# Optimization experiments

Measured on AMD Instinct MI355X. Metric: run time of the kernel, lower is better.

The kernel has to match this reference:

```python
import jax, jax.numpy as jnp
import numpy as np

PAD = 0
NEG_INF = -1e30

B, P, Q, D = 32, 4096, 64, 128  # batch, passage len, question len, nhid


def setup_inputs() -> dict:
    key = jax.random.key(0)
    k1, k2, k3, k4, k5, k6 = jax.random.split(key, 6)
    return {
        "tensor_H": jax.random.normal(k1, (B, P, D), dtype=jnp.float32),
        "tensor_U": jax.random.normal(k2, (B, Q, D), dtype=jnp.float32),
        "M": jax.random.normal(k3, (B, P, D), dtype=jnp.float32),
        "sentence_word_rep": jax.random.randint(k4, (B, P), 0, 10000, dtype=jnp.int64),
        "W_attn": jax.random.normal(k5, (D, D), dtype=jnp.float32) / np.sqrt(D),
        "W_cls": jax.random.normal(k6, (5 * D, 2), dtype=jnp.float32) / np.sqrt(5 * D),
    }


def reference(tensor_H, tensor_U, M, sentence_word_rep, W_attn, W_cls):
    # Matrix attention (bilinear): S[b,p,q] = h_p^T W u_q  -> (B, P, Q)
    S = jnp.einsum("bpd,de,bqe->bpq", tensor_H, W_attn, tensor_U)
    # context-to-query: softmax over question axis, then bmm with U
    c2q = jnp.einsum("bpq,bqd->bpd", jax.nn.softmax(S, axis=2), tensor_U)
    # query-to-context: softmax over passage axis of row-max, weighted sum of H
    b_attn = jax.nn.softmax(jnp.max(S, axis=2), axis=-1)        # (B, P)
    q2c = jnp.einsum("bp,bpd->bd", b_attn, tensor_H)[:, None, :]  # (B, 1, D) broadcast over P
    # G = [H; c2q; H*c2q; H*q2c] -> (B, P, 4D); G_M = [G; M] -> (B, P, 5D)
    G_M = jnp.concatenate(
        [tensor_H, c2q, tensor_H * c2q, tensor_H * q2c, M], axis=2
    )
    # masked max-pool over passage positions (mask where token == PAD)
    pad_mask = (sentence_word_rep == PAD)[:, :, None]           # (B, P, 1)
    pooled = jnp.max(jnp.where(pad_mask, NEG_INF, G_M), axis=1)  # (B, 5D)
    # final linear classifier (no bias)
    return pooled @ W_cls                                        # (B, 2)
```

## Files before the change

### kernel.cpp

```cpp
#include <hip/hip_runtime.h>

#define B_ 32
#define P_ 4096
#define Q_ 64
#define D_ 128

#define PART_STRIDE 772
#define NCHUNK 32
#define CHUNK_ROWS 128
#define TWS_BYTES (96*16384)

typedef __attribute__((ext_vector_type(8))) short bf16x8;
typedef __attribute__((ext_vector_type(4))) float f32x4;

__device__ __forceinline__ unsigned int asu(float x) { return __float_as_uint(x); }
__device__ __forceinline__ float asf(unsigned int x) { return __uint_as_float(x); }

__global__ __launch_bounds__(256) void k_T(const float* __restrict__ U,
                                           const float* __restrict__ W,
                                           char* __restrict__ Tws) {
  __shared__ float Wl[128*132];
  __shared__ float Ul[8*128];
  const int b = blockIdx.x >> 3, qc = blockIdx.x & 7;
  const int t = threadIdx.x;
#pragma unroll
  for (int k = 0; k < 16; ++k) {
    int i = t*4 + k*1024;
    float4 wv = *(const float4*)(W + i);
    int d = i >> 7, e = i & 127;
    *(float4*)(&Wl[d*132 + e]) = wv;
  }
  {
    int i = t*4;
    int q = i >> 7, e = i & 127;
    *(float4*)(&Ul[q*128 + e]) =
        *(const float4*)(U + ((size_t)(b*Q_ + qc*8 + q))*D_ + e);
  }
  __syncthreads();
  const int d = t & 127, qhalf = t >> 7;
  char* Thi = Tws + b*16384;
  char* Tlo = Tws + 32*16384 + b*16384;
  char* Utl = Tws + 64*16384 + b*16384;
#pragma unroll
  for (int pass = 0; pass < 4; ++pass) {
    const int ql = pass*2 + qhalf;
    const int qg = qc*8 + ql;
    float acc = 0.f;
#pragma unroll
    for (int e = 0; e < 128; e += 4) {
      float4 wv = *(float4*)(&Wl[d*132 + e]);
      float4 uv = *(float4*)(&Ul[ql*128 + e]);
      acc += wv.x*uv.x + wv.y*uv.y + wv.z*uv.z + wv.w*uv.w;
    }
    unsigned int au = asu(acc);
    unsigned short hs = (unsigned short)(au >> 16);
    float lo = acc - asf(au & 0xFFFF0000u);
    unsigned short ls = (unsigned short)(asu(lo) >> 16);
    int ta = (qg*256 + 2*d) ^ ((qg & 7) << 4);
    *(unsigned short*)(Thi + ta) = hs;
    *(unsigned short*)(Tlo + ta) = ls;
    float uval = Ul[ql*128 + d];
    int ua = (d*128 + 2*qg) ^ ((d & 7) << 4);
    *(unsigned short*)(Utl + ua) = (unsigned short)(asu(uval) >> 16);
  }
}

__global__ __launch_bounds__(512, 3) void k_main(
    const float* __restrict__ H, const float* __restrict__ M,
    const int* __restrict__ tok, const char* __restrict__ Tws,
    float* __restrict__ part) {
  __shared__ __align__(16) char Tl[32768];
  __shared__ __align__(16) char Pl[16384];
  __shared__ __align__(16) float mrow[128];
  __shared__ __align__(16) float rzrow[128];
  __shared__ __align__(16) float prow[128];
  __shared__ __align__(16) float bm[128];
  __shared__ int tkl[128];

  const int bid = blockIdx.x;
  const int b = bid >> 5, chunk = bid & 31;
  const int t = threadIdx.x, wv = t >> 6, l = t & 63;
  const int r15 = l & 15, g4 = l >> 4;
  const char* Thi_g = Tws + b*16384;
  const char* Tlo_g = Tws + 32*16384 + b*16384;
  const char* Utl   = Tws + 64*16384 + b*16384;

  const int dA = wv*16 + r15;
  bf16x8 au0 = *(const bf16x8*)(Utl + ((dA*128 + g4*16 +  0) ^ ((dA & 7) << 4)));
  bf16x8 au1 = *(const bf16x8*)(Utl + ((dA*128 + g4*16 + 64) ^ ((dA & 7) << 4)));

  {
    const uint4* sh = (const uint4*)Thi_g;
    const uint4* sl = (const uint4*)Tlo_g;
    uint4* dh = (uint4*)Tl;
    uint4* dl = (uint4*)(Tl + 16384);
    dh[t]       = sh[t];
    dh[t + 512] = sh[t + 512];
    dl[t]       = sl[t];
    dl[t + 512] = sl[t + 512];
  }
  if (t < 128) tkl[t] = tok[b*P_ + chunk*CHUNK_ROWS + t];
  __syncthreads();

  const int rowB = b*P_ + chunk*CHUNK_ROWS;

  {
    const int lrow0 = wv*16;
    const float* Arow = H + (size_t)(rowB + lrow0 + r15)*D_;
    f32x4 fA[4], fB[4];
#pragma unroll
    for (int ks = 0; ks < 4; ++ks) {
      const float* ap = Arow + ks*32 + g4*8;
      fA[ks] = *(const f32x4*)(ap);
      fB[ks] = *(const f32x4*)(ap + 4);
    }
    union { bf16x8 v; unsigned int u[4]; } Ah[4], Al[4];
#pragma unroll
    for (int ks = 0; ks < 4; ++ks) {
      unsigned int a0 = asu(fA[ks][0]), a1 = asu(fA[ks][1]),
                   a2 = asu(fA[ks][2]), a3 = asu(fA[ks][3]);
      unsigned int c0 = asu(fB[ks][0]), c1 = asu(fB[ks][1]),
                   c2 = asu(fB[ks][2]), c3 = asu(fB[ks][3]);
      Ah[ks].u[0] = (a1 & 0xFFFF0000u) | (a0 >> 16);
      Ah[ks].u[1] = (a3 & 0xFFFF0000u) | (a2 >> 16);
      Ah[ks].u[2] = (c1 & 0xFFFF0000u) | (c0 >> 16);
      Ah[ks].u[3] = (c3 & 0xFFFF0000u) | (c2 >> 16);
      float p0 = fA[ks][0] - asf(a0 & 0xFFFF0000u);
      float p1 = fA[ks][1] - asf(a1 & 0xFFFF0000u);
      float p2 = fA[ks][2] - asf(a2 & 0xFFFF0000u);
      float p3 = fA[ks][3] - asf(a3 & 0xFFFF0000u);
      float p4 = fB[ks][0] - asf(c0 & 0xFFFF0000u);
      float p5 = fB[ks][1] - asf(c1 & 0xFFFF0000u);
      float p6 = fB[ks][2] - asf(c2 & 0xFFFF0000u);
      float p7 = fB[ks][3] - asf(c3 & 0xFFFF0000u);
      Al[ks].u[0] = (asu(p1) & 0xFFFF0000u) | (asu(p0) >> 16);
      Al[ks].u[1] = (asu(p3) & 0xFFFF0000u) | (asu(p2) >> 16);
      Al[ks].u[2] = (asu(p5) & 0xFFFF0000u) | (asu(p4) >> 16);
      Al[ks].u[3] = (asu(p7) & 0xFFFF0000u) | (asu(p6) >> 16);
    }
    f32x4 sacc[4];
#pragma unroll
    for (int qt = 0; qt < 4; ++qt) sacc[qt] = (f32x4){0.f, 0.f, 0.f, 0.f};
#pragma unroll
    for (int ks = 0; ks < 4; ++ks) {
#pragma unroll
      for (int qt = 0; qt < 4; ++qt) {
        int q = qt*16 + r15;
        int off = (q*256 + ks*64 + g4*16) ^ ((q & 7) << 4);
        bf16x8 bh = *(const bf16x8*)(Tl + off);
        bf16x8 bl = *(const bf16x8*)(Tl + 16384 + off);
        sacc[qt] = __builtin_amdgcn_mfma_f32_16x16x32_bf16(Al[ks].v, bh, sacc[qt], 0, 0, 0);
        sacc[qt] = __builtin_amdgcn_mfma_f32_16x16x32_bf16(Ah[ks].v, bl, sacc[qt], 0, 0, 0);
        sacc[qt] = __builtin_amdgcn_mfma_f32_16x16x32_bf16(Ah[ks].v, bh, sacc[qt], 0, 0, 0);
      }
    }
    float m[4];
#pragma unroll
    for (int j = 0; j < 4; ++j)
      m[j] = fmaxf(fmaxf(sacc[0][j], sacc[1][j]), fmaxf(sacc[2][j], sacc[3][j]));
#pragma unroll
    for (int off = 1; off <= 8; off <<= 1)
#pragma unroll
      for (int j = 0; j < 4; ++j) m[j] = fmaxf(m[j], __shfl_xor(m[j], off));
    float Zp[4] = {0.f, 0.f, 0.f, 0.f};
#pragma unroll
    for (int qt = 0; qt < 4; ++qt)
#pragma unroll
      for (int j = 0; j < 4; ++j) {
        float e = __expf(sacc[qt][j] - m[j]);
        Zp[j] += e;
        int p = lrow0 + g4*4 + j, q = qt*16 + r15;
        int off = (p*128 + 2*q) ^ ((p & 7) << 4);
        *(unsigned short*)(Pl + off) = (unsigned short)(asu(e) >> 16);
      }
#pragma unroll
    for (int off = 1; off <= 8; off <<= 1)
#pragma unroll
      for (int j = 0; j < 4; ++j) Zp[j] += __shfl_xor(Zp[j], off);
    if (r15 == 0) {
#pragma unroll
      for (int j = 0; j < 4; ++j) {
        mrow[lrow0 + g4*4 + j]  = m[j];
        rzrow[lrow0 + g4*4 + j] = __builtin_amdgcn_rcpf(Zp[j]);
      }
    }
  }
  __syncthreads();

  float m0 = mrow[l], m1 = mrow[l + 64];
  float Lm = fmaxf(m0, m1);
#pragma unroll
  for (int off = 1; off <= 32; off <<= 1) Lm = fmaxf(Lm, __shfl_xor(Lm, off));
  float ssum = __expf(m0 - Lm) + __expf(m1 - Lm);
#pragma unroll
  for (int off = 1; off <= 32; off <<= 1) ssum += __shfl_xor(ssum, off);
  if (t < 128) {
    prow[t] = __expf(mrow[t] - Lm);
    bm[t]   = tkl[t] ? 0.f : -1.0e38f;
  }
  __syncthreads();

  f32x4 v4  = (f32x4){0.f, 0.f, 0.f, 0.f};
  f32x4 xH4 = (f32x4){-3.0e38f, -3.0e38f, -3.0e38f, -3.0e38f};
  f32x4 nH4 = (f32x4){ 3.0e38f,  3.0e38f,  3.0e38f,  3.0e38f};
  f32x4 xC4 = (f32x4){-3.0e38f, -3.0e38f, -3.0e38f, -3.0e38f};
  f32x4 xHC4= (f32x4){-3.0e38f, -3.0e38f, -3.0e38f, -3.0e38f};
  f32x4 xM4 = (f32x4){-3.0e38f, -3.0e38f, -3.0e38f, -3.0e38f};
  const int dbase = wv*16 + g4*4;
#pragma unroll
  for (int rti = 0; rti < 8; ++rti) {
    const int rt = (rti + wv) & 7;
    const int p = rt*16 + r15;
    const int pswz = (p & 7) << 4;
    bf16x8 pb0 = *(bf16x8*)(Pl + ((p*128 + g4*16 +  0) ^ pswz));
    bf16x8 pb1 = *(bf16x8*)(Pl + ((p*128 + g4*16 + 64) ^ pswz));
    f32x4 pv = (f32x4){0.f, 0.f, 0.f, 0.f};
    pv = __builtin_amdgcn_mfma_f32_16x16x32_bf16(au0, pb0, pv, 0, 0, 0);
    pv = __builtin_amdgcn_mfma_f32_16x16x32_bf16(au1, pb1, pv, 0, 0, 0);
    const float prw = prow[p], rz = rzrow[p], bmv = bm[p];
    f32x4 h4 = *(const f32x4*)(H + (size_t)(rowB + p)*D_ + dbase);
    f32x4 m4 = *(const f32x4*)(M + (size_t)(rowB + p)*D_ + dbase);
#pragma unroll
    for (int j = 0; j < 4; ++j) {
      float c = pv[j] * rz;
      v4[j]   += prw*h4[j];
      xH4[j]   = fmaxf(xH4[j],  h4[j] + bmv);
      nH4[j]   = fminf(nH4[j],  h4[j] - bmv);
      xC4[j]   = fmaxf(xC4[j],  c + bmv);
      xHC4[j]  = fmaxf(xHC4[j], h4[j]*c + bmv);
      xM4[j]   = fmaxf(xM4[j],  m4[j] + bmv);
    }
  }
#pragma unroll
  for (int off = 1; off <= 8; off <<= 1) {
#pragma unroll
    for (int j = 0; j < 4; ++j) {
      v4[j]  += __shfl_xor(v4[j], off);
      xH4[j]  = fmaxf(xH4[j],  __shfl_xor(xH4[j],  off));
      nH4[j]  = fminf(nH4[j],  __shfl_xor(nH4[j],  off));
      xC4[j]  = fmaxf(xC4[j],  __shfl_xor(xC4[j],  off));
      xHC4[j] = fmaxf(xHC4[j], __shfl_xor(xHC4[j], off));
      xM4[j]  = fmaxf(xM4[j],  __shfl_xor(xM4[j],  off));
    }
  }
  float* pp = part + (size_t)bid*PART_STRIDE;
  if (t == 0) { pp[0] = Lm; pp[1] = ssum; }
  if (r15 == 0) {
#pragma unroll
    for (int j = 0; j < 4; ++j) {
      pp[2 + dbase + j]   = v4[j];
      pp[130 + dbase + j] = xH4[j];
      pp[258 + dbase + j] = nH4[j];
      pp[386 + dbase + j] = xC4[j];
      pp[514 + dbase + j] = xHC4[j];
      pp[642 + dbase + j] = xM4[j];
    }
  }
}

__global__ __launch_bounds__(128) void k_final(const float* __restrict__ part,
                                               const float* __restrict__ Wc,
                                               float* __restrict__ out) {
  __shared__ float pooled[640];
  __shared__ float r0s[2], r1s[2];
  const int b = blockIdx.x, t = threadIdx.x;
  const float* pb = part + (size_t)b*NCHUNK*PART_STRIDE;
  float L = -3.0e38f;
#pragma unroll
  for (int c = 0; c < NCHUNK; ++c) L = fmaxf(L, pb[c*PART_STRIDE]);
  float S = 0.f, V = 0.f;
  float mh = -3.0e38f, nh = 3.0e38f, mc = -3.0e38f, mhc = -3.0e38f, mm = -3.0e38f;
#pragma unroll
  for (int c = 0; c < NCHUNK; ++c) {
    const float* p = pb + c*PART_STRIDE;
    float e = __expf(p[0] - L);
    S += p[1]*e;
    V += p[2 + t]*e;
    mh  = fmaxf(mh,  p[130 + t]);
    nh  = fminf(nh,  p[258 + t]);
    mc  = fmaxf(mc,  p[386 + t]);
    mhc = fmaxf(mhc, p[514 + t]);
    mm  = fmaxf(mm,  p[642 + t]);
  }
  float q2c = V / S;
  pooled[t]       = mh;
  pooled[128 + t] = mc;
  pooled[256 + t] = mhc;
  pooled[384 + t] = (q2c >= 0.f) ? q2c*mh : q2c*nh;
  pooled[512 + t] = mm;
  __syncthreads();
  float a0 = 0.f, a1 = 0.f;
#pragma unroll
  for (int k = t; k < 640; k += 128) {
    float pv = pooled[k];
    a0 += pv*Wc[k*2 + 0];
    a1 += pv*Wc[k*2 + 1];
  }
#pragma unroll
  for (int off = 32; off; off >>= 1) {
    a0 += __shfl_xor(a0, off);
    a1 += __shfl_xor(a1, off);
  }
  if ((t & 63) == 0) { r0s[t >> 6] = a0; r1s[t >> 6] = a1; }
  __syncthreads();
  if (t == 0) {
    out[b*2 + 0] = r0s[0] + r0s[1];
    out[b*2 + 1] = r1s[0] + r1s[1];
  }
}

extern "C" void kernel_launch(void* const* d_in, const int* in_sizes, int n_in,
                              void* d_out, int out_size, void* d_ws, size_t ws_size,
                              hipStream_t stream) {
  const float* H   = (const float*)d_in[0];
  const float* U   = (const float*)d_in[1];
  const float* M   = (const float*)d_in[2];
  const int*   tok = (const int*)d_in[3];
  const float* Wa  = (const float*)d_in[4];
  const float* Wc  = (const float*)d_in[5];
  float* out = (float*)d_out;
  char* wsc = (char*)d_ws;
  char* Tws = wsc;
  float* part = (float*)(wsc + TWS_BYTES);

  hipLaunchKernelGGL(k_T,     dim3(256),        dim3(256), 0, stream, U, Wa, Tws);
  hipLaunchKernelGGL(k_main,  dim3(B_*NCHUNK),  dim3(512), 0, stream, H, M, tok, Tws, part);
  hipLaunchKernelGGL(k_final, dim3(B_),         dim3(128), 0, stream, part, Wc, out);
}
```

Before: 58.89 us.

## Process two 128-row halves per block to amortize T staging

Doubles the rows handled by each main-kernel block from 128 to 256, so there are half as many blocks. Each block stages the per-batch T matrix into LDS once and runs two interleaved 128-row streams through the MFMA score, softmax and pooling phases. This amortizes the T load and block setup and raises instruction-level parallelism per wave. In exchange it uses more registers and LDS, drops the occupancy hint from 3 to 2 blocks per CU, and launches fewer blocks (512 instead of 1024).

```diff
diff --git a/kernel.cpp b/kernel.cpp
--- a/kernel.cpp
+++ b/kernel.cpp
@@ -6,8 +6,8 @@
 #define D_ 128
 
 #define PART_STRIDE 772
-#define NCHUNK 32
-#define CHUNK_ROWS 128
+#define NCHUNK 16
+#define CHUNK_ROWS 256
 #define TWS_BYTES (96*16384)
 
 typedef __attribute__((ext_vector_type(8))) short bf16x8;
@@ -15,6 +15,30 @@
 
 __device__ __forceinline__ unsigned int asu(float x) { return __float_as_uint(x); }
 __device__ __forceinline__ float asf(unsigned int x) { return __uint_as_float(x); }
+
+__device__ __forceinline__ void repack8(const f32x4 fa, const f32x4 fb,
+                                        bf16x8* hi, bf16x8* lo) {
+  union { bf16x8 v; unsigned int u[4]; } Hh, Ll;
+  unsigned int a0 = asu(fa[0]), a1 = asu(fa[1]), a2 = asu(fa[2]), a3 = asu(fa[3]);
+  unsigned int c0 = asu(fb[0]), c1 = asu(fb[1]), c2 = asu(fb[2]), c3 = asu(fb[3]);
+  Hh.u[0] = (a1 & 0xFFFF0000u) | (a0 >> 16);
+  Hh.u[1] = (a3 & 0xFFFF0000u) | (a2 >> 16);
+  Hh.u[2] = (c1 & 0xFFFF0000u) | (c0 >> 16);
+  Hh.u[3] = (c3 & 0xFFFF0000u) | (c2 >> 16);
+  float p0 = fa[0] - asf(a0 & 0xFFFF0000u);
+  float p1 = fa[1] - asf(a1 & 0xFFFF0000u);
+  float p2 = fa[2] - asf(a2 & 0xFFFF0000u);
+  float p3 = fa[3] - asf(a3 & 0xFFFF0000u);
+  float p4 = fb[0] - asf(c0 & 0xFFFF0000u);
+  float p5 = fb[1] - asf(c1 & 0xFFFF0000u);
+  float p6 = fb[2] - asf(c2 & 0xFFFF0000u);
+  float p7 = fb[3] - asf(c3 & 0xFFFF0000u);
+  Ll.u[0] = (asu(p1) & 0xFFFF0000u) | (asu(p0) >> 16);
+  Ll.u[1] = (asu(p3) & 0xFFFF0000u) | (asu(p2) >> 16);
+  Ll.u[2] = (asu(p5) & 0xFFFF0000u) | (asu(p4) >> 16);
+  Ll.u[3] = (asu(p7) & 0xFFFF0000u) | (asu(p6) >> 16);
+  *hi = Hh.v; *lo = Ll.v;
+}
 
 __global__ __launch_bounds__(256) void k_T(const float* __restrict__ U,
                                            const float* __restrict__ W,
@@ -65,20 +89,21 @@
   }
 }
 
-__global__ __launch_bounds__(512, 3) void k_main(
+__global__ __launch_bounds__(512, 2) void k_main(
     const float* __restrict__ H, const float* __restrict__ M,
     const int* __restrict__ tok, const char* __restrict__ Tws,
     float* __restrict__ part) {
   __shared__ __align__(16) char Tl[32768];
-  __shared__ __align__(16) char Pl[16384];
-  __shared__ __align__(16) float mrow[128];
-  __shared__ __align__(16) float rzrow[128];
-  __shared__ __align__(16) float prow[128];
-  __shared__ __align__(16) float bm[128];
-  __shared__ int tkl[128];
+  __shared__ __align__(16) char PA[16384];
+  __shared__ __align__(16) char PB[16384];
+  __shared__ __align__(16) float mrow[256];
+  __shared__ __align__(16) float rzrow[256];
+  __shared__ __align__(16) float prow[256];
+  __shared__ __align__(16) float bm[256];
+  __shared__ int tkl[256];
 
   const int bid = blockIdx.x;
-  const int b = bid >> 5, chunk = bid & 31;
+  const int b = bid >> 4, chunk = bid & 15;
   const int t = threadIdx.x, wv = t >> 6, l = t & 63;
   const int r15 = l & 15, g4 = l >> 4;
   const char* Thi_g = Tws + b*16384;
@@ -99,48 +124,37 @@
     dl[t]       = sl[t];
     dl[t + 512] = sl[t + 512];
   }
-  if (t < 128) tkl[t] = tok[b*P_ + chunk*CHUNK_ROWS + t];
+  if (t < 256) tkl[t] = tok[b*P_ + chunk*CHUNK_ROWS + t];
   __syncthreads();
 
   const int rowB = b*P_ + chunk*CHUNK_ROWS;
 
   {
     const int lrow0 = wv*16;
-    const float* Arow = H + (size_t)(rowB + lrow0 + r15)*D_;
-    f32x4 fA[4], fB[4];
+    const float* ArowA = H + (size_t)(rowB + lrow0 + r15)*D_;
+    const float* ArowB = H + (size_t)(rowB + 128 + lrow0 + r15)*D_;
+    f32x4 fa0[4], fb0[4], fa1[4], fb1[4];
 #pragma unroll
     for (int ks = 0; ks < 4; ++ks) {
-      const float* ap = Arow + ks*32 + g4*8;
-      fA[ks] = *(const f32x4*)(ap);
-      fB[ks] = *(const f32x4*)(ap + 4);
-    }
-    union { bf16x8 v; unsigned int u[4]; } Ah[4], Al[4];
+      const float* apA = ArowA + ks*32 + g4*8;
+      const float* apB = ArowB + ks*32 + g4*8;
+      fa0[ks] = *(const f32x4*)(apA);
+      fb0[ks] = *(const f32x4*)(apA + 4);
+      fa1[ks] = *(const f32x4*)(apB);
+      fb1[ks] = *(const f32x4*)(apB + 4);
+    }
+    bf16x8 AhA[4], AlA[4], AhB[4], AlB[4];
 #pragma unroll
     for (int ks = 0; ks < 4; ++ks) {
-      unsigned int a0 = asu(fA[ks][0]), a1 = asu(fA[ks][1]),
-                   a2 = asu(fA[ks][2]), a3 = asu(fA[ks][3]);
-      unsigned int c0 = asu(fB[ks][0]), c1 = asu(fB[ks][1]),
-                   c2 = asu(fB[ks][2]), c3 = asu(fB[ks][3]);
-      Ah[ks].u[0] = (a1 & 0xFFFF0000u) | (a0 >> 16);
-      Ah[ks].u[1] = (a3 & 0xFFFF0000u) | (a2 >> 16);
-      Ah[ks].u[2] = (c1 & 0xFFFF0000u) | (c0 >> 16);
-      Ah[ks].u[3] = (c3 & 0xFFFF0000u) | (c2 >> 16);
-      float p0 = fA[ks][0] - asf(a0 & 0xFFFF0000u);
-      float p1 = fA[ks][1] - asf(a1 & 0xFFFF0000u);
-      float p2 = fA[ks][2] - asf(a2 & 0xFFFF0000u);
-      float p3 = fA[ks][3] - asf(a3 & 0xFFFF0000u);
-      float p4 = fB[ks][0] - asf(c0 & 0xFFFF0000u);
-      float p5 = fB[ks][1] - asf(c1 & 0xFFFF0000u);
-      float p6 = fB[ks][2] - asf(c2 & 0xFFFF0000u);
-      float p7 = fB[ks][3] - asf(c3 & 0xFFFF0000u);
-      Al[ks].u[0] = (asu(p1) & 0xFFFF0000u) | (asu(p0) >> 16);
-      Al[ks].u[1] = (asu(p3) & 0xFFFF0000u) | (asu(p2) >> 16);
-      Al[ks].u[2] = (asu(p5) & 0xFFFF0000u) | (asu(p4) >> 16);
-      Al[ks].u[3] = (asu(p7) & 0xFFFF0000u) | (asu(p6) >> 16);
-    }
-    f32x4 sacc[4];
-#pragma unroll
-    for (int qt = 0; qt < 4; ++qt) sacc[qt] = (f32x4){0.f, 0.f, 0.f, 0.f};
+      repack8(fa0[ks], fb0[ks], &AhA[ks], &AlA[ks]);
+      repack8(fa1[ks], fb1[ks], &AhB[ks], &AlB[ks]);
+    }
+    f32x4 sA[4], sB[4];
+#pragma unroll
+    for (int qt = 0; qt < 4; ++qt) {
+      sA[qt] = (f32x4){0.f, 0.f, 0.f, 0.f};
+      sB[qt] = (f32x4){0.f, 0.f, 0.f, 0.f};
+    }
 #pragma unroll
     for (int ks = 0; ks < 4; ++ks) {
 #pragma unroll
@@ -149,52 +163,68 @@
         int off = (q*256 + ks*64 + g4*16) ^ ((q & 7) << 4);
         bf16x8 bh = *(const bf16x8*)(Tl + off);
         bf16x8 bl = *(const bf16x8*)(Tl + 16384 + off);
-        sacc[qt] = __builtin_amdgcn_mfma_f32_16x16x32_bf16(Al[ks].v, bh, sacc[qt], 0, 0, 0);
-        sacc[qt] = __builtin_amdgcn_mfma_f32_16x16x32_bf16(Ah[ks].v, bl, sacc[qt], 0, 0, 0);
-        sacc[qt] = __builtin_amdgcn_mfma_f32_16x16x32_bf16(Ah[ks].v, bh, sacc[qt], 0, 0, 0);
-      }
-    }
-    float m[4];
-#pragma unroll
-    for (int j = 0; j < 4; ++j)
-      m[j] = fmaxf(fmaxf(sacc[0][j], sacc[1][j]), fmaxf(sacc[2][j], sacc[3][j]));
+        sA[qt] = __builtin_amdgcn_mfma_f32_16x16x32_bf16(AlA[ks], bh, sA[qt], 0, 0, 0);
+        sA[qt] = __builtin_amdgcn_mfma_f32_16x16x32_bf16(AhA[ks], bl, sA[qt], 0, 0, 0);
+        sA[qt] = __builtin_amdgcn_mfma_f32_16x16x32_bf16(AhA[ks], bh, sA[qt], 0, 0, 0);
+        sB[qt] = __builtin_amdgcn_mfma_f32_16x16x32_bf16(AlB[ks], bh, sB[qt], 0, 0, 0);
+        sB[qt] = __builtin_amdgcn_mfma_f32_16x16x32_bf16(AhB[ks], bl, sB[qt], 0, 0, 0);
+        sB[qt] = __builtin_amdgcn_mfma_f32_16x16x32_bf16(AhB[ks], bh, sB[qt], 0, 0, 0);
+      }
+    }
+    float mA[4], mB[4];
+#pragma unroll
+    for (int j = 0; j < 4; ++j) {
+      mA[j] = fmaxf(fmaxf(sA[0][j], sA[1][j]), fmaxf(sA[2][j], sA[3][j]));
+      mB[j] = fmaxf(fmaxf(sB[0][j], sB[1][j]), fmaxf(sB[2][j], sB[3][j]));
+    }
 #pragma unroll
     for (int off = 1; off <= 8; off <<= 1)
 #pragma unroll
-      for (int j = 0; j < 4; ++j) m[j] = fmaxf(m[j], __shfl_xor(m[j], off));
-    float Zp[4] = {0.f, 0.f, 0.f, 0.f};
+      for (int j = 0; j < 4; ++j) {
+        mA[j] = fmaxf(mA[j], __shfl_xor(mA[j], off));
+        mB[j] = fmaxf(mB[j], __shfl_xor(mB[j], off));
+      }
+    float ZA[4] = {0.f,0.f,0.f,0.f}, ZB[4] = {0.f,0.f,0.f,0.f};
 #pragma unroll
     for (int qt = 0; qt < 4; ++qt)
 #pragma unroll
       for (int j = 0; j < 4; ++j) {
-        float e = __expf(sacc[qt][j] - m[j]);
-        Zp[j] += e;
+        float eA = __expf(sA[qt][j] - mA[j]);
+        float eB = __expf(sB[qt][j] - mB[j]);
+        ZA[j] += eA;
+        ZB[j] += eB;
         int p = lrow0 + g4*4 + j, q = qt*16 + r15;
         int off = (p*128 + 2*q) ^ ((p & 7) << 4);
-        *(unsigned short*)(Pl + off) = (unsigned short)(asu(e) >> 16);
+        *(unsigned short*)(PA + off) = (unsigned short)(asu(eA) >> 16);
+        *(unsigned short*)(PB + off) = (unsigned short)(asu(eB) >> 16);
       }
 #pragma unroll
     for (int off = 1; off <= 8; off <<= 1)
 #pragma unroll
-      for (int j = 0; j < 4; ++j) Zp[j] += __shfl_xor(Zp[j], off);
+      for (int j = 0; j < 4; ++j) {
+        ZA[j] += __shfl_xor(ZA[j], off);
+        ZB[j] += __shfl_xor(ZB[j], off);
+      }
     if (r15 == 0) {
 #pragma unroll
       for (int j = 0; j < 4; ++j) {
-        mrow[lrow0 + g4*4 + j]  = m[j];
-        rzrow[lrow0 + g4*4 + j] = __builtin_amdgcn_rcpf(Zp[j]);
-      }
-    }
-  }
-  __syncthreads();
-
-  float m0 = mrow[l], m1 = mrow[l + 64];
-  float Lm = fmaxf(m0, m1);
+        mrow[lrow0 + g4*4 + j]        = mA[j];
+        rzrow[lrow0 + g4*4 + j]       = __builtin_amdgcn_rcpf(ZA[j]);
+        mrow[128 + lrow0 + g4*4 + j]  = mB[j];
+        rzrow[128 + lrow0 + g4*4 + j] = __builtin_amdgcn_rcpf(ZB[j]);
+      }
+    }
+  }
+  __syncthreads();
+
+  float q0 = mrow[l], q1 = mrow[l + 64], q2 = mrow[l + 128], q3 = mrow[l + 192];
+  float Lm = fmaxf(fmaxf(q0, q1), fmaxf(q2, q3));
 #pragma unroll
   for (int off = 1; off <= 32; off <<= 1) Lm = fmaxf(Lm, __shfl_xor(Lm, off));
-  float ssum = __expf(m0 - Lm) + __expf(m1 - Lm);
+  float ssum = __expf(q0 - Lm) + __expf(q1 - Lm) + __expf(q2 - Lm) + __expf(q3 - Lm);
 #pragma unroll
   for (int off = 1; off <= 32; off <<= 1) ssum += __shfl_xor(ssum, off);
-  if (t < 128) {
+  if (t < 256) {
     prow[t] = __expf(mrow[t] - Lm);
     bm[t]   = tkl[t] ? 0.f : -1.0e38f;
   }
@@ -210,25 +240,34 @@
 #pragma unroll
   for (int rti = 0; rti < 8; ++rti) {
     const int rt = (rti + wv) & 7;
-    const int p = rt*16 + r15;
-    const int pswz = (p & 7) << 4;
-    bf16x8 pb0 = *(bf16x8*)(Pl + ((p*128 + g4*16 +  0) ^ pswz));
-    bf16x8 pb1 = *(bf16x8*)(Pl + ((p*128 + g4*16 + 64) ^ pswz));
-    f32x4 pv = (f32x4){0.f, 0.f, 0.f, 0.f};
-    pv = __builtin_amdgcn_mfma_f32_16x16x32_bf16(au0, pb0, pv, 0, 0, 0);
-    pv = __builtin_amdgcn_mfma_f32_16x16x32_bf16(au1, pb1, pv, 0, 0, 0);
-    const float prw = prow[p], rz = rzrow[p], bmv = bm[p];
-    f32x4 h4 = *(const f32x4*)(H + (size_t)(rowB + p)*D_ + dbase);
-    f32x4 m4 = *(const f32x4*)(M + (size_t)(rowB + p)*D_ + dbase);
+    const int pl = rt*16 + r15;
+    const int pswz = (pl & 7) << 4;
+    bf16x8 pa0 = *(bf16x8*)(PA + ((pl*128 + g4*16 +  0) ^ pswz));
+    bf16x8 pa1 = *(bf16x8*)(PA + ((pl*128 + g4*16 + 64) ^ pswz));
+    bf16x8 pbb0 = *(bf16x8*)(PB + ((pl*128 + g4*16 +  0) ^ pswz));
+    bf16x8 pbb1 = *(bf16x8*)(PB + ((pl*128 + g4*16 + 64) ^ pswz));
+    f32x4 pvA = (f32x4){0.f, 0.f, 0.f, 0.f};
+    f32x4 pvB = (f32x4){0.f, 0.f, 0.f, 0.f};
+    pvA = __builtin_amdgcn_mfma_f32_16x16x32_bf16(au0, pa0, pvA, 0, 0, 0);
+    pvA = __builtin_amdgcn_mfma_f32_16x16x32_bf16(au1, pa1, pvA, 0, 0, 0);
+    pvB = __builtin_amdgcn_mfma_f32_16x16x32_bf16(au0, pbb0, pvB, 0, 0, 0);
+    pvB = __builtin_amdgcn_mfma_f32_16x16x32_bf16(au1, pbb1, pvB, 0, 0, 0);
+    const float prA = prow[pl],       rzA = rzrow[pl],       bmA = bm[pl];
+    const float prB = prow[128 + pl], rzB = rzrow[128 + pl], bmB = bm[128 + pl];
+    f32x4 h4a = *(const f32x4*)(H + (size_t)(rowB + pl)*D_ + dbase);
+    f32x4 m4a = *(const f32x4*)(M + (size_t)(rowB + pl)*D_ + dbase);
+    f32x4 h4b = *(const f32x4*)(H + (size_t)(rowB + 128 + pl)*D_ + dbase);
+    f32x4 m4b = *(const f32x4*)(M + (size_t)(rowB + 128 + pl)*D_ + dbase);
 #pragma unroll
     for (int j = 0; j < 4; ++j) {
-      float c = pv[j] * rz;
-      v4[j]   += prw*h4[j];
-      xH4[j]   = fmaxf(xH4[j],  h4[j] + bmv);
-      nH4[j]   = fminf(nH4[j],  h4[j] - bmv);
-      xC4[j]   = fmaxf(xC4[j],  c + bmv);
-      xHC4[j]  = fmaxf(xHC4[j], h4[j]*c + bmv);
-      xM4[j]   = fmaxf(xM4[j],  m4[j] + bmv);
+      float cA = pvA[j] * rzA;
+      float cB = pvB[j] * rzB;
+      v4[j]   += prA*h4a[j] + prB*h4b[j];
+      xH4[j]   = fmaxf(xH4[j],  fmaxf(h4a[j] + bmA, h4b[j] + bmB));
+      nH4[j]   = fminf(nH4[j],  fminf(h4a[j] - bmA, h4b[j] - bmB));
+      xC4[j]   = fmaxf(xC4[j],  fmaxf(cA + bmA, cB + bmB));
+      xHC4[j]  = fmaxf(xHC4[j], fmaxf(h4a[j]*cA + bmA, h4b[j]*cB + bmB));
+      xM4[j]   = fmaxf(xM4[j],  fmaxf(m4a[j] + bmA, m4b[j] + bmB));
     }
   }
 #pragma unroll
```

Measured after the change: 61.84 us. 5.0% more time.
